# Kernel tuning notes

Hardware: AMD Instinct MI355X
Metric: run time of the kernel (lower is better)

Reference implementation:

```python
import jax, jax.numpy as jnp
import numpy as np
import math

STRIDE = ((2, 2), (4, 4), (8, 8), (16, 16))  # (ws, hs) pairs
D_MODEL = 256
B, H, W = 8, 128, 128
BN_EPS = 1e-5
LEAKY_SLOPE = 0.2


def setup_inputs() -> dict:
    key = jax.random.key(0)
    ks = jax.random.split(key, 8)
    s = 1.0 / math.sqrt(D_MODEL)
    s3 = 1.0 / math.sqrt(D_MODEL * 9)
    return {
        "x": jax.random.normal(ks[0], (B, D_MODEL, H, W), jnp.float32),
        "wq": jax.random.normal(ks[1], (D_MODEL, D_MODEL, 1, 1), jnp.float32) * s,
        "bq": jnp.zeros((D_MODEL,), jnp.float32),
        "wk": jax.random.normal(ks[2], (D_MODEL, D_MODEL, 1, 1), jnp.float32) * s,
        "bk": jnp.zeros((D_MODEL,), jnp.float32),
        "wv": jax.random.normal(ks[3], (D_MODEL, D_MODEL, 1, 1), jnp.float32) * s,
        "bv": jnp.zeros((D_MODEL,), jnp.float32),
        "wo": jax.random.normal(ks[4], (D_MODEL, D_MODEL, 3, 3), jnp.float32) * s3,
        "bo": jnp.zeros((D_MODEL,), jnp.float32),
        "gamma": jnp.ones((D_MODEL,), jnp.float32),
        "beta": jnp.zeros((D_MODEL,), jnp.float32),
    }


def _conv1x1(x, w, bias):
    # 1x1 conv == channel matmul
    return jnp.einsum('bchw,oc->bohw', x, w[:, :, 0, 0]) + bias[None, :, None, None]


def reference(x, wq, bq, wk, bk, wv, bv, wo, bo, gamma, beta):
    b, c, h, w = x.shape
    n = len(STRIDE)
    d_k = c // n
    q = _conv1x1(x, wq, bq)
    k = _conv1x1(x, wk, bk)
    v = _conv1x1(x, wv, bv)
    outs = []
    for idx, (ws, hs) in enumerate(STRIDE):
        lo = idx * d_k
        oh, ow = h // hs, w // ws

        def gather(t):
            # strided patch gather: element (i,j) head <- t[:, :, i::hs, j::ws]
            t = t[:, lo:lo + d_k].reshape(b, d_k, oh, hs, ow, ws)
            return t.transpose(0, 3, 5, 1, 2, 4).reshape(b, hs * ws, d_k * oh * ow)

        qi, ki, vi = gather(q), gather(k), gather(v)
        scale = 1.0 / jnp.sqrt(jnp.asarray(qi.shape[-1], qi.dtype))
        scores = jnp.einsum('bsd,btd->bst', qi, ki) * scale  # [b, hs*ws, hs*ws]
        p = jax.nn.softmax(scores, axis=-1)
        y = jnp.einsum('bst,btd->bsd', p, vi)
        # scatter back exactly as the torch permute(0,3,1,4,2,5): h = i*oh + row
        y = y.reshape(b, hs, ws, d_k, oh, ow).transpose(0, 3, 1, 4, 2, 5).reshape(b, d_k, h, w)
        outs.append(y)
    out = jnp.concatenate(outs, axis=1)  # [b, c, h, w]
    # output_linear: 3x3 conv -> BatchNorm2d (training-mode batch stats) -> LeakyReLU(0.2)
    out = jax.lax.conv_general_dilated(out, wo, (1, 1), 'SAME',
                                       dimension_numbers=('NCHW', 'OIHW', 'NCHW'))
    out = out + bo[None, :, None, None]
    mean = out.mean(axis=(0, 2, 3))
    var = out.var(axis=(0, 2, 3))
    out = (out - mean[None, :, None, None]) * jax.lax.rsqrt(var[None, :, None, None] + BN_EPS)
    out = out * gamma[None, :, None, None] + beta[None, :, None, None]
    return jnp.where(out > 0, out, LEAKY_SLOPE * out)
```

## Files before the change

kernel.cpp:

```cpp
#include <hip/hip_runtime.h>
#include <stdint.h>


#define DEVI static __device__ __forceinline__

typedef short bf8 __attribute__((ext_vector_type(8)));
typedef float f32x4 __attribute__((ext_vector_type(4)));

DEVI unsigned short f2bf(float f) {
  unsigned u = __builtin_bit_cast(unsigned, f);
  u = (u + 0x7fffu + ((u >> 16) & 1u)) >> 16;
  return (unsigned short)u;
}
DEVI float bf2f(unsigned short h) {
  unsigned u = ((unsigned)h) << 16;
  return __builtin_bit_cast(float, u);
}

DEVI void gload16(const void* g, void* l) {
  __builtin_amdgcn_global_load_lds(
      (const __attribute__((address_space(1))) unsigned int*)g,
      (__attribute__((address_space(3))) unsigned int*)l, 16, 0, 0);
}

static const size_t WB_OFF  = 0;
static const size_t WOB_OFF = 393216;
static const size_t QN_OFF  = 1572864;
static const size_t KN_OFF  = QN_OFF + 67108864;
static const size_t VN_OFF  = KN_OFF + 67108864;
static const size_t YN_OFF  = VN_OFF + 67108864;
static const size_t SC_OFF  = YN_OFF + 67108864;
static const size_t PRB_OFF = SC_OFF + 2236928;
static const size_t BNP_OFF = PRB_OFF + 1118464;
static const size_t BNS_OFF = BNP_OFF + 4194304;
static const size_t ZP_OFF  = BNS_OFF + 2048;
static const size_t WS_NEED = ZP_OFF + 256;

__global__ void k_prep(const float* __restrict__ wq, const float* __restrict__ wk,
                       const float* __restrict__ wv, const float* __restrict__ wo,
                       unsigned short* __restrict__ Wb, unsigned short* __restrict__ Wob) {
  int i = blockIdx.x * 256 + threadIdx.x;
  if (i < 196608) {
    int z = i >> 16, r = i & 65535;
    const float* w = (z == 0) ? wq : (z == 1) ? wk : wv;
    Wb[i] = f2bf(w[r]);
  } else {
    int j = i - 196608;
    int o = j / 2304, k = j - o * 2304;
    int e = k >> 8, c = k & 255;
    Wob[j] = f2bf(wo[(o * 256 + c) * 9 + e]);
  }
}

__global__ void k_zero(float* __restrict__ p, int n) {
  int i = blockIdx.x * 256 + threadIdx.x;
  for (; i < n; i += gridDim.x * 256) p[i] = 0.f;
}

__global__ __launch_bounds__(256) void k_qkv(
    const float* __restrict__ x, const unsigned short* __restrict__ Wb,
    const float* __restrict__ bq, const float* __restrict__ bk, const float* __restrict__ bv,
    unsigned short* __restrict__ Qn, unsigned short* __restrict__ Kn,
    unsigned short* __restrict__ Vn) {
  const int pt = blockIdx.x, b = blockIdx.y;
  const int p0 = pt * 64;
  const int tid = threadIdx.x;

  __shared__ __align__(16) unsigned short xt[64 * 256];
  __shared__ __align__(16) unsigned short ot[64 * 256];

  const float* xb = x + (size_t)b * 256 * 16384;
  for (int k = 0; k < 16; ++k) {
    int i = tid + k * 256;
    int c = i >> 4, p4 = (i & 15) * 4;
    float4 v = *(const float4*)(xb + (size_t)c * 16384 + p0 + p4);
    xt[(p4 + 0) * 256 + (c ^ (((p4 + 0) & 7) << 3))] = f2bf(v.x);
    xt[(p4 + 1) * 256 + (c ^ (((p4 + 1) & 7) << 3))] = f2bf(v.y);
    xt[(p4 + 2) * 256 + (c ^ (((p4 + 2) & 7) << 3))] = f2bf(v.z);
    xt[(p4 + 3) * 256 + (c ^ (((p4 + 3) & 7) << 3))] = f2bf(v.w);
  }
  __syncthreads();

  const int wave = tid >> 6, lane = tid & 63;
  const int lr = lane & 15, lk = lane >> 4;
  const int obase = wave * 64;

  for (int z = 0; z < 3; ++z) {
    const unsigned short* Wz = Wb + (size_t)z * 65536;
    f32x4 acc[4][4];
    for (int m = 0; m < 4; ++m)
      for (int n = 0; n < 4; ++n)
        for (int r = 0; r < 4; ++r) acc[m][n][r] = 0.f;

    for (int ks = 0; ks < 8; ++ks) {
      int c0 = ks * 32 + lk * 8;
      bf8 a[4], bb[4];
#pragma unroll
      for (int m = 0; m < 4; ++m)
        a[m] = *(const bf8*)(Wz + (size_t)(obase + m * 16 + lr) * 256 + c0);
#pragma unroll
      for (int n = 0; n < 4; ++n) {
        int p = n * 16 + lr;
        bb[n] = *(const bf8*)(&xt[p * 256 + (c0 ^ ((p & 7) << 3))]);
      }
#pragma unroll
      for (int m = 0; m < 4; ++m)
#pragma unroll
        for (int n = 0; n < 4; ++n)
          acc[m][n] = __builtin_amdgcn_mfma_f32_16x16x32_bf16(a[m], bb[n], acc[m][n], 0, 0, 0);
    }

    const float* bias = (z == 0) ? bq : (z == 1) ? bk : bv;
    unsigned short* On = (z == 0) ? Qn : (z == 1) ? Kn : Vn;
    __syncthreads();
#pragma unroll
    for (int m = 0; m < 4; ++m) {
      int ob4 = obase + m * 16 + lk * 4;
      float4 b4 = *(const float4*)(bias + ob4);
#pragma unroll
      for (int n = 0; n < 4; ++n) {
        int p = n * 16 + lr;
        ushort4 v4;
        v4.x = f2bf(acc[m][n][0] + b4.x);
        v4.y = f2bf(acc[m][n][1] + b4.y);
        v4.z = f2bf(acc[m][n][2] + b4.z);
        v4.w = f2bf(acc[m][n][3] + b4.w);
        *(ushort4*)(&ot[p * 256 + (ob4 ^ ((p & 7) << 3))]) = v4;
      }
    }
    __syncthreads();
    unsigned short* gb = On + ((size_t)b * 16384 + p0) * 256;
#pragma unroll
    for (int i = 0; i < 8; ++i) {
      int ch = tid + i * 256;
      *(uint4*)(gb + ch * 8) = *(const uint4*)(&ot[ch * 8]);
    }
  }
}

template <int IDX>
__global__ __launch_bounds__(256) void k_gram(
    const unsigned short* __restrict__ Qn, const unsigned short* __restrict__ Kn,
    float* __restrict__ scores) {
  constexpr int HS = 2 << IDX, S = HS * HS, OH = 64 >> IDX, NSP = OH * OH;
  constexpr int SPW = (IDX == 2) ? 2 : 8;
  constexpr int DSUB = SPW * 64;
  constexpr int SPB = NSP / 32;
  constexpr int STEPS = SPB / SPW;
  constexpr int ROWS = S;
  constexpr int TPT = S * SPW * 8 / 256;
  constexpr int SCOFF = (IDX == 0) ? 0 : (IDX == 1) ? 128 : 2176;
  constexpr int HC = IDX * 64;
  constexpr int MT = (IDX == 2) ? 4 : 1;

  const int chk = blockIdx.x, b = blockIdx.y;
  const int tid = threadIdx.x;
  const int wave = tid >> 6, lane = tid & 63, lr = lane & 15, lk = lane >> 4;

  __shared__ __align__(16) unsigned short qg[ROWS * DSUB];
  __shared__ __align__(16) unsigned short kg[ROWS * DSUB];
  __shared__ float red[S * S];

  const size_t base = (size_t)b * 16384 * 256;

  f32x4 acc[MT][MT];
  for (int m = 0; m < MT; ++m)
    for (int n = 0; n < MT; ++n)
      for (int r = 0; r < 4; ++r) acc[m][n][r] = 0.f;

  for (int st = 0; st < STEPS; ++st) {
    const int sp0 = chk * SPB + st * SPW;
    __syncthreads();
#pragma unroll
    for (int r = 0; r < TPT; ++r) {
      int task = tid + r * 256;
      int cg = task & 7, pl = task >> 3;
      int spl = pl >> (2 * (IDX + 1)), s = pl & (S - 1);
      int sp = sp0 + spl;
      int ohi = sp >> (6 - IDX), owi = sp & (OH - 1);
      int ii = s >> (IDX + 1), jj = s & (HS - 1);
      int p = (ohi * HS + ii) * 128 + owi * HS + jj;
      size_t gaddr = base + (size_t)p * 256 + HC + ((cg ^ (p & 7)) << 3);
      int laddr = s * DSUB + (((spl * 8 + cg) ^ (s & 7)) << 3);
      *(uint4*)(qg + laddr) = *(const uint4*)(Qn + gaddr);
      *(uint4*)(kg + laddr) = *(const uint4*)(Kn + gaddr);
    }
    __syncthreads();
    if (IDX == 2) {
      int kgid = wave * 4 + lk;
      bf8 a[4], bb[4];
#pragma unroll
      for (int m = 0; m < 4; ++m) {
        int row = m * 16 + lr;
        int off = row * DSUB + ((kgid ^ (row & 7)) << 3);
        a[m] = *(const bf8*)(qg + off);
        bb[m] = *(const bf8*)(kg + off);
      }
#pragma unroll
      for (int m = 0; m < 4; ++m)
#pragma unroll
        for (int n = 0; n < 4; ++n)
          acc[m][n] = __builtin_amdgcn_mfma_f32_16x16x32_bf16(a[m], bb[n], acc[m][n], 0, 0, 0);
    } else {
      int row = lr & (ROWS - 1);
#pragma unroll
      for (int kk = 0; kk < 4; ++kk) {
        int kgid = (wave * 4 + kk) * 4 + lk;
        int off = row * DSUB + ((kgid ^ (row & 7)) << 3);
        bf8 a = *(const bf8*)(qg + off);
        bf8 bb = *(const bf8*)(kg + off);
        acc[0][0] = __builtin_amdgcn_mfma_f32_16x16x32_bf16(a, bb, acc[0][0], 0, 0, 0);
      }
    }
  }

  __syncthreads();
  for (int i2 = tid; i2 < S * S; i2 += 256) red[i2] = 0.f;
  __syncthreads();
  if (IDX == 2) {
#pragma unroll
    for (int m = 0; m < 4; ++m)
#pragma unroll
      for (int n = 0; n < 4; ++n)
#pragma unroll
        for (int r = 0; r < 4; ++r)
          atomicAdd(&red[(m * 16 + lk * 4 + r) * 64 + n * 16 + lr], acc[m][n][r]);
  } else if (IDX == 1) {
#pragma unroll
    for (int r = 0; r < 4; ++r)
      atomicAdd(&red[(lk * 4 + r) * 16 + lr], acc[0][0][r]);
  } else {
    if (lk == 0 && lr < 4) {
#pragma unroll
      for (int r = 0; r < 4; ++r)
        atomicAdd(&red[r * 4 + lr], acc[0][0][r]);
    }
  }
  __syncthreads();
  float* sc = scores + SCOFF + (size_t)b * S * S;
  for (int i2 = tid; i2 < S * S; i2 += 256) atomicAdd(sc + i2, red[i2]);
}

__global__ __launch_bounds__(256) void k_gram3(
    const unsigned short* __restrict__ Qn, const unsigned short* __restrict__ Kn,
    float* __restrict__ part3) {
  const int qc = blockIdx.x, tq = blockIdx.y, b = blockIdx.z;
  const int tid = threadIdx.x;
  const int wave = tid >> 6, lane = tid & 63, lr = lane & 15, lk = lane >> 4;

  __shared__ __align__(16) unsigned short qg[256 * 64];
  __shared__ __align__(16) unsigned short kg[64 * 64];

  const size_t base = (size_t)b * 16384 * 256;

  f32x4 acc[4][4];
  for (int m = 0; m < 4; ++m)
    for (int n = 0; n < 4; ++n)
      for (int r = 0; r < 4; ++r) acc[m][n][r] = 0.f;

  for (int st = 0; st < 8; ++st) {
    int sp = qc * 8 + st;
    int ohi = sp >> 3, owi = sp & 7;
    __syncthreads();
#pragma unroll
    for (int r = 0; r < 8; ++r) {
      int task = tid + r * 256;
      int cg = task & 7, s = task >> 3;
      int p = (ohi * 16 + (s >> 4)) * 128 + owi * 16 + (s & 15);
      uint4 v = *(const uint4*)(Qn + base + (size_t)p * 256 + 192 + ((cg ^ (p & 7)) << 3));
      *(uint4*)(qg + s * 64 + ((cg ^ (s & 7)) << 3)) = v;
    }
#pragma unroll
    for (int r = 0; r < 2; ++r) {
      int task = tid + r * 256;
      int cg = task & 7, tl = task >> 3;
      int p = (ohi * 16 + tq * 4 + (tl >> 4)) * 128 + owi * 16 + (tl & 15);
      uint4 v = *(const uint4*)(Kn + base + (size_t)p * 256 + 192 + ((cg ^ (p & 7)) << 3));
      *(uint4*)(kg + tl * 64 + ((cg ^ (tl & 7)) << 3)) = v;
    }
    __syncthreads();
#pragma unroll
    for (int kk = 0; kk < 2; ++kk) {
      int kgid = kk * 4 + lk;
      bf8 a[4], bb[4];
#pragma unroll
      for (int m = 0; m < 4; ++m) {
        int row = wave * 64 + m * 16 + lr;
        a[m] = *(const bf8*)(qg + row * 64 + ((kgid ^ (row & 7)) << 3));
      }
#pragma unroll
      for (int n = 0; n < 4; ++n) {
        int rowb = n * 16 + lr;
        bb[n] = *(const bf8*)(kg + rowb * 64 + ((kgid ^ (rowb & 7)) << 3));
      }
#pragma unroll
      for (int m = 0; m < 4; ++m)
#pragma unroll
        for (int n = 0; n < 4; ++n)
          acc[m][n] = __builtin_amdgcn_mfma_f32_16x16x32_bf16(a[m], bb[n], acc[m][n], 0, 0, 0);
    }
  }

  float* pb = part3 + (((size_t)qc * 8 + b) * 65536);
#pragma unroll
  for (int m = 0; m < 4; ++m)
#pragma unroll
    for (int r = 0; r < 4; ++r) {
      int srow = wave * 64 + m * 16 + lk * 4 + r;
#pragma unroll
      for (int n = 0; n < 4; ++n)
        pb[srow * 256 + tq * 64 + n * 16 + lr] = acc[m][n][r];
    }
}

__global__ __launch_bounds__(256) void k_softmax(const float* __restrict__ scores,
                                                 unsigned short* __restrict__ prb) {
  const int idx = blockIdx.x, b = blockIdx.y;
  const int S = 4 << (2 * idx);
  const int off = (idx == 0 ? 0 : idx == 1 ? 128 : 2176) + b * S * S;
  const int s = threadIdx.x;
  if (s >= S) return;
  const float scale = rsqrtf(64.0f * (float)(4096 >> (2 * idx)));
  const float* row = scores + off + s * S;
  float m = -1e30f;
  for (int t = 0; t < S; ++t) m = fmaxf(m, row[t]);
  m *= scale;
  float sum = 0.f;
  for (int t = 0; t < S; ++t) sum += __expf(row[t] * scale - m);
  float inv = 1.0f / sum;
  unsigned short* prow = prb + off + s * S;
  for (int t = 0; t < S; ++t) prow[t] = f2bf(__expf(row[t] * scale - m) * inv);
}

__global__ __launch_bounds__(256) void k_softmax3(const float* __restrict__ part3,
                                                  unsigned short* __restrict__ prb) {
  const int sc_ = blockIdx.x, b = blockIdx.y;
  const int tid = threadIdx.x;
  const int s = sc_ * 32 + (tid >> 3);
  const int t0 = (tid & 7) * 32;
  float v[32];
#pragma unroll
  for (int k = 0; k < 32; ++k) v[k] = 0.f;
  for (int q = 0; q < 8; ++q) {
    const float4* pp = (const float4*)(part3 + (((size_t)q * 8 + b) * 256 + s) * 256 + t0);
#pragma unroll
    for (int k = 0; k < 8; ++k) {
      float4 u = pp[k];
      v[k * 4 + 0] += u.x; v[k * 4 + 1] += u.y; v[k * 4 + 2] += u.z; v[k * 4 + 3] += u.w;
    }
  }
  const float scale = 1.0f / 64.0f;
  float m = -1e30f;
#pragma unroll
  for (int k = 0; k < 32; ++k) { v[k] *= scale; m = fmaxf(m, v[k]); }
  m = fmaxf(m, __shfl_xor(m, 1));
  m = fmaxf(m, __shfl_xor(m, 2));
  m = fmaxf(m, __shfl_xor(m, 4));
  float sum = 0.f;
#pragma unroll
  for (int k = 0; k < 32; ++k) { v[k] = __expf(v[k] - m); sum += v[k]; }
  sum += __shfl_xor(sum, 1);
  sum += __shfl_xor(sum, 2);
  sum += __shfl_xor(sum, 4);
  float inv = 1.0f / sum;
  unsigned short* prw = prb + 34944 + (size_t)b * 65536 + s * 256 + t0;
#pragma unroll
  for (int k8 = 0; k8 < 4; ++k8) {
    unsigned short tmp[8];
#pragma unroll
    for (int e = 0; e < 8; ++e) tmp[e] = f2bf(v[k8 * 8 + e] * inv);
    *(uint4*)(prw + k8 * 8) = *(const uint4*)tmp;
  }
}

template <int IDX>
__global__ __launch_bounds__(256) void k_pv(
    const unsigned short* __restrict__ Vn, const unsigned short* __restrict__ prb,
    unsigned short* __restrict__ Yn) {
  constexpr int HS = 2 << IDX, S = HS * HS, OH = 64 >> IDX;
  constexpr int IT = (IDX == 0) ? 8 : (IDX == 1) ? 4 : 1;
  constexpr int POFF = (IDX == 0) ? 0 : (IDX == 1) ? 128 : 2176;
  const int bx = blockIdx.x, b = blockIdx.y;
  const int c = threadIdx.x & 63, spg = threadIdx.x >> 6;
  __shared__ __align__(16) float pl[S * S];
  const unsigned short* pr = prb + POFF + (size_t)b * S * S;
  for (int i = threadIdx.x; i < S * S; i += 256) pl[i] = bf2f(pr[i]);
  __syncthreads();
  const int hc = IDX * 64;
  const unsigned short* vb = Vn + (size_t)b * 16384 * 256;
  unsigned short* yb = Yn + (size_t)b * 16384 * 256;
  for (int it = 0; it < IT; ++it) {
    int sp = bx * (4 * IT) + it * 4 + spg;
    int ohi = sp >> (6 - IDX), owi = sp & (OH - 1);
    float v[S];
#pragma unroll
    for (int t = 0; t < S; ++t) {
      int po = (ohi * HS + t / HS) * 128 + owi * HS + (t % HS);
      v[t] = bf2f(vb[(size_t)po * 256 + ((hc + c) ^ ((po & 7) << 3))]);
    }
    for (int s = 0; s < S; ++s) {
      const float4* p4 = (const float4*)(pl + s * S);
      float a = 0.f;
#pragma unroll
      for (int t4 = 0; t4 < S / 4; ++t4) {
        float4 pp = p4[t4];
        a += pp.x * v[t4 * 4] + pp.y * v[t4 * 4 + 1] + pp.z * v[t4 * 4 + 2] + pp.w * v[t4 * 4 + 3];
      }
      int po = ((s >> (IDX + 1)) * OH + ohi) * 128 + (s & (HS - 1)) * OH + owi;
      yb[(size_t)po * 256 + ((hc + c) ^ ((po & 7) << 3))] = f2bf(a);
    }
  }
}

__global__ __launch_bounds__(256) void k_pv3(
    const unsigned short* __restrict__ Vn, const unsigned short* __restrict__ prb,
    unsigned short* __restrict__ Yn) {
  const int sp = blockIdx.x, b = blockIdx.y;
  const int ohi = sp >> 3, owi = sp & 7;
  const int tid = threadIdx.x;
  __shared__ __align__(16) unsigned short vl[64 * 256];
  const unsigned short* vb = Vn + (size_t)b * 16384 * 256;
  {
    int t = tid;
    int po = (ohi * 16 + (t >> 4)) * 128 + owi * 16 + (t & 15);
    const unsigned short* src = vb + (size_t)po * 256;
    int xv = (po & 7) << 3;
#pragma unroll
    for (int g = 0; g < 8; ++g) {
      ushort4 lo = *(const ushort4*)(src + ((192 + g * 8) ^ xv));
      ushort4 hi = *(const ushort4*)(src + ((192 + g * 8) ^ xv) + 4);
      unsigned short vv[8] = {lo.x, lo.y, lo.z, lo.w, hi.x, hi.y, hi.z, hi.w};
#pragma unroll
      for (int e = 0; e < 8; ++e) {
        int cc = g * 8 + e;
        vl[cc * 256 + (t ^ ((cc & 7) << 3))] = vv[e];
      }
    }
  }
  __syncthreads();

  const int wave = tid >> 6, lane = tid & 63;
  const int lr = lane & 15, lk = lane >> 4;
  const int sb = wave * 64;
  const unsigned short* pr = prb + 34944 + (size_t)b * 65536;

  f32x4 acc[4][4];
  for (int m = 0; m < 4; ++m)
    for (int n = 0; n < 4; ++n)
      for (int r = 0; r < 4; ++r) acc[m][n][r] = 0.f;

  for (int kk = 0; kk < 8; ++kk) {
    int t0 = kk * 32 + lk * 8;
    bf8 a[4], bb[4];
#pragma unroll
    for (int m = 0; m < 4; ++m)
      a[m] = *(const bf8*)(pr + (size_t)(sb + m * 16 + lr) * 256 + t0);
#pragma unroll
    for (int n = 0; n < 4; ++n) {
      int cc = n * 16 + lr;
      bb[n] = *(const bf8*)(&vl[cc * 256 + (t0 ^ ((cc & 7) << 3))]);
    }
#pragma unroll
    for (int m = 0; m < 4; ++m)
#pragma unroll
      for (int n = 0; n < 4; ++n)
        acc[m][n] = __builtin_amdgcn_mfma_f32_16x16x32_bf16(a[m], bb[n], acc[m][n], 0, 0, 0);
  }

  unsigned short* yb = Yn + (size_t)b * 16384 * 256;
#pragma unroll
  for (int m = 0; m < 4; ++m) {
#pragma unroll
    for (int r = 0; r < 4; ++r) {
      int s = sb + m * 16 + lk * 4 + r;
      int si = s >> 4, sj = s & 15;
      int po = (si * 8 + ohi) * 128 + sj * 8 + owi;
#pragma unroll
      for (int n = 0; n < 4; ++n) {
        int cc = 192 + n * 16 + lr;
        yb[(size_t)po * 256 + (cc ^ (owi << 3))] = f2bf(acc[m][n][r]);
      }
    }
  }
}

__global__ __launch_bounds__(512, 2) void k_conv(
    const unsigned short* __restrict__ Yn, const unsigned short* __restrict__ Wob,
    const float* __restrict__ bo, const unsigned short* __restrict__ zp,
    float* __restrict__ out, float* __restrict__ bnp) {
  __shared__ __align__(16) unsigned short ldsA[2][16384];
  __shared__ __align__(16) unsigned short ldsB[2][16384];

  const int bid = blockIdx.x;
  const int swz = (bid & 7) * 64 + (bid >> 3);
  const int b = swz >> 6, tile = swz & 63;
  const int y0 = (tile >> 3) * 16, x0 = (tile & 7) * 16;
  const int tid = threadIdx.x;
  const int wave = tid >> 6, lane = tid & 63;
  const int lr = lane & 15, lk = lane >> 4;
  const int wm = wave >> 2, wn = wave & 3;

  const unsigned short* yb = Yn + (size_t)b * 16384 * 256;

  auto STAGE = [&](int buf, int st) {
    int e = st >> 2;
    int dy = e / 3 - 1, dx = e % 3 - 1;
    int c0 = (st & 3) * 64, g0 = (st & 3) * 8;
#pragma unroll
    for (int i = 0; i < 4; ++i) {
      int task = (wave * 4 + i) * 64 + lane;
      int o = task >> 3, cg = task & 7;
      const unsigned short* sa = Wob + o * 2304 + e * 256 + c0 + ((cg ^ (o & 7)) << 3);
      gload16(sa, &ldsA[buf][(wave * 4 + i) * 512]);
      int py = o >> 4, px = o & 15;
      int h = y0 + py + dy, w = x0 + px + dx;
      const unsigned short* sb;
      if (h >= 0 && h < 128 && w >= 0 && w < 128) {
        int pp = h * 128 + w;
        int gl = (cg ^ (o & 7)) ^ (pp & 7);
        sb = yb + (size_t)pp * 256 + ((g0 + gl) << 3);
      } else {
        sb = zp;
      }
      gload16(sb, &ldsB[buf][(wave * 4 + i) * 512]);
    }
  };

  f32x4 acc[8][4];
#pragma unroll
  for (int m = 0; m < 8; ++m)
#pragma unroll
    for (int n = 0; n < 4; ++n)
#pragma unroll
      for (int r = 0; r < 4; ++r) acc[m][n][r] = 0.f;

  int cur = 0;
  STAGE(0, 0);
  for (int t = 0; t < 36; ++t) {
    if (t < 35) {
      STAGE(cur ^ 1, t + 1);
      asm volatile("s_waitcnt vmcnt(8)" ::: "memory");
    } else {
      asm volatile("s_waitcnt vmcnt(0)" ::: "memory");
    }
    __builtin_amdgcn_s_barrier();
    asm volatile("" ::: "memory");
#pragma unroll
    for (int kk = 0; kk < 2; ++kk) {
      int kg = kk * 4 + lk;
      bf8 a[8], bf[4];
#pragma unroll
      for (int m = 0; m < 8; ++m) {
        int row = wm * 128 + m * 16 + lr;
        a[m] = *(const bf8*)(&ldsA[cur][row * 64 + ((kg ^ (row & 7)) << 3)]);
      }
#pragma unroll
      for (int n = 0; n < 4; ++n) {
        int rn = wn * 64 + n * 16 + lr;
        bf[n] = *(const bf8*)(&ldsB[cur][rn * 64 + ((kg ^ (rn & 7)) << 3)]);
      }
#pragma unroll
      for (int m = 0; m < 8; ++m)
#pragma unroll
        for (int n = 0; n < 4; ++n)
          acc[m][n] = __builtin_amdgcn_mfma_f32_16x16x32_bf16(a[m], bf[n], acc[m][n], 0, 0, 0);
    }
    asm volatile("" ::: "memory");
    __builtin_amdgcn_s_barrier();
    cur ^= 1;
  }

  float* ob = out + (size_t)b * 256 * 16384;
  float* red1 = (float*)&ldsA[0][0];
  float* red2 = red1 + 1024;
#pragma unroll
  for (int m = 0; m < 8; ++m) {
#pragma unroll
    for (int r = 0; r < 4; ++r) {
      int o = wm * 128 + m * 16 + lk * 4 + r;
      float bvv = bo[o];
      float s1 = 0.f, s2 = 0.f;
#pragma unroll
      for (int n = 0; n < 4; ++n) {
        int pix = wn * 64 + n * 16 + lr;
        int py = pix >> 4, px = pix & 15;
        float v = acc[m][n][r] + bvv;
        ob[(size_t)o * 16384 + (y0 + py) * 128 + x0 + px] = v;
        s1 += v;
        s2 += v * v;
      }
      for (int off = 1; off < 16; off <<= 1) {
        s1 += __shfl_xor(s1, off, 64);
        s2 += __shfl_xor(s2, off, 64);
      }
      if (lr == 0) {
        int ol = m * 16 + lk * 4 + r;
        red1[wave * 128 + ol] = s1;
        red2[wave * 128 + ol] = s2;
      }
    }
  }
  __syncthreads();
  {
    int o = tid & 255, stat = tid >> 8;
    int wm2 = o >> 7, ol = o & 127;
    const float* rd = stat ? red2 : red1;
    float s = rd[(wm2 * 4 + 0) * 128 + ol] + rd[(wm2 * 4 + 1) * 128 + ol] +
              rd[(wm2 * 4 + 2) * 128 + ol] + rd[(wm2 * 4 + 3) * 128 + ol];
    bnp[((size_t)(b * 64 + tile) * 256 + o) * 2 + stat] = s;
  }
}

__global__ __launch_bounds__(256) void k_bnred(
    const float* __restrict__ bnp, const float* __restrict__ gamma,
    const float* __restrict__ beta, float* __restrict__ bns) {
  const int o = blockIdx.x;
  const int tid = threadIdx.x;
  float s1 = 0.f, s2 = 0.f;
  for (int k = tid; k < 512; k += 256) {
    s1 += bnp[((size_t)k * 256 + o) * 2 + 0];
    s2 += bnp[((size_t)k * 256 + o) * 2 + 1];
  }
  __shared__ float r1[256], r2[256];
  r1[tid] = s1; r2[tid] = s2;
  __syncthreads();
  for (int off = 128; off > 0; off >>= 1) {
    if (tid < off) { r1[tid] += r1[tid + off]; r2[tid] += r2[tid + off]; }
    __syncthreads();
  }
  if (tid == 0) {
    const float cnt = 8.0f * 16384.0f;
    float mean = r1[0] / cnt;
    float var = r2[0] / cnt - mean * mean;
    float sc = gamma[o] * rsqrtf(var + 1e-5f);
    bns[o] = sc;
    bns[256 + o] = beta[o] - mean * sc;
  }
}

__global__ void k_bnapply(float* __restrict__ out, const float* __restrict__ bns) {
  size_t i = ((size_t)blockIdx.x * 256 + threadIdx.x) * 4;
  const size_t total = 33554432;
  const size_t stride = (size_t)gridDim.x * 256 * 4;
  for (; i < total; i += stride) {
    float4 v = *(float4*)(out + i);
    int o = (int)((i >> 14) & 255);
    float sc = bns[o], shv = bns[256 + o];
    v.x = v.x * sc + shv; v.x = v.x > 0.f ? v.x : 0.2f * v.x;
    v.y = v.y * sc + shv; v.y = v.y > 0.f ? v.y : 0.2f * v.y;
    v.z = v.z * sc + shv; v.z = v.z > 0.f ? v.z : 0.2f * v.z;
    v.w = v.w * sc + shv; v.w = v.w > 0.f ? v.w : 0.2f * v.w;
    *(float4*)(out + i) = v;
  }
}

extern "C" void kernel_launch(void* const* d_in, const int* in_sizes, int n_in,
                              void* d_out, int out_size, void* d_ws, size_t ws_size,
                              hipStream_t stream) {
  if (ws_size < WS_NEED) return;

  const float* x     = (const float*)d_in[0];
  const float* wq    = (const float*)d_in[1];
  const float* bq    = (const float*)d_in[2];
  const float* wk    = (const float*)d_in[3];
  const float* bk    = (const float*)d_in[4];
  const float* wv    = (const float*)d_in[5];
  const float* bv    = (const float*)d_in[6];
  const float* wo    = (const float*)d_in[7];
  const float* bo    = (const float*)d_in[8];
  const float* gamma = (const float*)d_in[9];
  const float* beta  = (const float*)d_in[10];
  float* out = (float*)d_out;
  char* ws = (char*)d_ws;

  unsigned short* Wb  = (unsigned short*)(ws + WB_OFF);
  unsigned short* Wob = (unsigned short*)(ws + WOB_OFF);
  unsigned short* Qn  = (unsigned short*)(ws + QN_OFF);
  unsigned short* Kn  = (unsigned short*)(ws + KN_OFF);
  unsigned short* Vn  = (unsigned short*)(ws + VN_OFF);
  unsigned short* Yn  = (unsigned short*)(ws + YN_OFF);
  float* part3 = (float*)(ws + YN_OFF);
  float* scores = (float*)(ws + SC_OFF);
  unsigned short* prb = (unsigned short*)(ws + PRB_OFF);
  float* bnp    = (float*)(ws + BNP_OFF);
  float* bns    = (float*)(ws + BNS_OFF);
  unsigned short* zp = (unsigned short*)(ws + ZP_OFF);

  k_prep<<<dim3(3072), dim3(256), 0, stream>>>(wq, wk, wv, wo, Wb, Wob);
  k_zero<<<dim3(137), dim3(256), 0, stream>>>(scores, 34944);
  k_zero<<<dim3(1), dim3(64), 0, stream>>>((float*)zp, 64);
  k_qkv<<<dim3(256, 8), dim3(256), 0, stream>>>(x, Wb, bq, bk, bv, Qn, Kn, Vn);
  k_gram<0><<<dim3(32, 8), dim3(256), 0, stream>>>(Qn, Kn, scores);
  k_gram<1><<<dim3(32, 8), dim3(256), 0, stream>>>(Qn, Kn, scores);
  k_gram<2><<<dim3(32, 8), dim3(256), 0, stream>>>(Qn, Kn, scores);
  k_gram3<<<dim3(8, 4, 8), dim3(256), 0, stream>>>(Qn, Kn, part3);
  k_softmax<<<dim3(3, 8), dim3(256), 0, stream>>>(scores, prb);
  k_softmax3<<<dim3(8, 8), dim3(256), 0, stream>>>(part3, prb);
  k_pv<0><<<dim3(128, 8), dim3(256), 0, stream>>>(Vn, prb, Yn);
  k_pv<1><<<dim3(64, 8), dim3(256), 0, stream>>>(Vn, prb, Yn);
  k_pv<2><<<dim3(64, 8), dim3(256), 0, stream>>>(Vn, prb, Yn);
  k_pv3<<<dim3(64, 8), dim3(256), 0, stream>>>(Vn, prb, Yn);
  k_conv<<<dim3(512), dim3(512), 0, stream>>>(Yn, Wob, bo, zp, out, bnp);
  k_bnred<<<dim3(256), dim3(256), 0, stream>>>(bnp, gamma, beta, bns);
  k_bnapply<<<dim3(4096), dim3(256), 0, stream>>>(out, bns);
}
```

Before: 613.3 us.

## Split conv K-tiles into quarter sub-tiles with an 8-slot LDS ring pipeline

Restructures the 3x3 conv GEMM main loop. The old double-buffered 256x256x64 stage is split into four half-tile LDS slots (two A halves, two B halves) inside an 8-slot ring, with loads issued five sub-stages ahead. Each sub-step computes one quadrant of the accumulator tile, and MFMA sections are wrapped in s_setprio. The aim is to deepen prefetch and overlap global-to-LDS loads with MFMA at finer granularity, at the cost of more barriers per K-step and more complex bookkeeping.

```diff
diff --git a/kernel.cpp b/kernel.cpp
--- a/kernel.cpp
+++ b/kernel.cpp
@@ -488,8 +488,7 @@
     const unsigned short* __restrict__ Yn, const unsigned short* __restrict__ Wob,
     const float* __restrict__ bo, const unsigned short* __restrict__ zp,
     float* __restrict__ out, float* __restrict__ bnp) {
-  __shared__ __align__(16) unsigned short ldsA[2][16384];
-  __shared__ __align__(16) unsigned short ldsB[2][16384];
+  __shared__ __align__(16) unsigned short lds[8][8192];
 
   const int bid = blockIdx.x;
   const int swz = (bid & 7) * 64 + (bid >> 3);
@@ -499,30 +498,36 @@
   const int wave = tid >> 6, lane = tid & 63;
   const int lr = lane & 15, lk = lane >> 4;
   const int wm = wave >> 2, wn = wave & 3;
+  const int cg = lane & 7;
 
   const unsigned short* yb = Yn + (size_t)b * 16384 * 256;
 
-  auto STAGE = [&](int buf, int st) {
-    int e = st >> 2;
-    int dy = e / 3 - 1, dx = e % 3 - 1;
-    int c0 = (st & 3) * 64, g0 = (st & 3) * 8;
-#pragma unroll
-    for (int i = 0; i < 4; ++i) {
-      int task = (wave * 4 + i) * 64 + lane;
-      int o = task >> 3, cg = task & 7;
-      const unsigned short* sa = Wob + o * 2304 + e * 256 + c0 + ((cg ^ (o & 7)) << 3);
-      gload16(sa, &ldsA[buf][(wave * 4 + i) * 512]);
-      int py = o >> 4, px = o & 15;
-      int h = y0 + py + dy, w = x0 + px + dx;
-      const unsigned short* sb;
-      if (h >= 0 && h < 128 && w >= 0 && w < 128) {
-        int pp = h * 128 + w;
-        int gl = (cg ^ (o & 7)) ^ (pp & 7);
-        sb = yb + (size_t)pp * 256 + ((g0 + gl) << 3);
-      } else {
-        sb = zp;
-      }
-      gload16(sb, &ldsB[buf][(wave * 4 + i) * 512]);
+  auto STAGE = [&](int slot, int w, int KT) {
+    if (w < 2) {
+      const unsigned short* wsrc = Wob + (KT >> 2) * 256 + (KT & 3) * 64;
+#pragma unroll
+      for (int j = 0; j < 2; ++j) {
+        int rp = (wave * 2 + j) * 8 + (lane >> 3);
+        int o = ((rp >> 6) & 1) * 128 + w * 64 + (rp & 63);
+        int kg = cg ^ (rp & 7);
+        gload16(wsrc + o * 2304 + (kg << 3), &lds[slot][(wave * 2 + j) * 512]);
+      }
+    } else {
+      int e = KT >> 2;
+      int dy = e / 3 - 1, dx = e % 3 - 1, c8 = (KT & 3) * 8;
+#pragma unroll
+      for (int j = 0; j < 2; ++j) {
+        int rp = (wave * 2 + j) * 8 + (lane >> 3);
+        int n = ((rp >> 5) & 3) * 64 + (w - 2) * 32 + (rp & 31);
+        int kg = cg ^ (rp & 7);
+        int h = y0 + (n >> 4) + dy, ww = x0 + (n & 15) + dx;
+        const unsigned short* src = zp;
+        if (h >= 0 && h < 128 && ww >= 0 && ww < 128) {
+          int pp = h * 128 + ww;
+          src = yb + (size_t)pp * 256 + ((c8 + (kg ^ (pp & 7))) << 3);
+        }
+        gload16(src, &lds[slot][(wave * 2 + j) * 512]);
+      }
     }
   };
 
@@ -534,44 +539,57 @@
 #pragma unroll
       for (int r = 0; r < 4; ++r) acc[m][n][r] = 0.f;
 
-  int cur = 0;
-  STAGE(0, 0);
-  for (int t = 0; t < 36; ++t) {
-    if (t < 35) {
-      STAGE(cur ^ 1, t + 1);
-      asm volatile("s_waitcnt vmcnt(8)" ::: "memory");
-    } else {
-      asm volatile("s_waitcnt vmcnt(0)" ::: "memory");
-    }
-    __builtin_amdgcn_s_barrier();
-    asm volatile("" ::: "memory");
-#pragma unroll
-    for (int kk = 0; kk < 2; ++kk) {
-      int kg = kk * 4 + lk;
-      bf8 a[8], bf[4];
-#pragma unroll
-      for (int m = 0; m < 8; ++m) {
-        int row = wm * 128 + m * 16 + lr;
-        a[m] = *(const bf8*)(&ldsA[cur][row * 64 + ((kg ^ (row & 7)) << 3)]);
-      }
-#pragma unroll
-      for (int n = 0; n < 4; ++n) {
-        int rn = wn * 64 + n * 16 + lr;
-        bf[n] = *(const bf8*)(&ldsB[cur][rn * 64 + ((kg ^ (rn & 7)) << 3)]);
-      }
-#pragma unroll
-      for (int m = 0; m < 8; ++m)
-#pragma unroll
-        for (int n = 0; n < 4; ++n)
-          acc[m][n] = __builtin_amdgcn_mfma_f32_16x16x32_bf16(a[m], bf[n], acc[m][n], 0, 0, 0);
-    }
-    asm volatile("" ::: "memory");
-    __builtin_amdgcn_s_barrier();
-    cur ^= 1;
-  }
-
+  STAGE(0, 0, 0); STAGE(1, 1, 0); STAGE(2, 2, 0); STAGE(3, 3, 0); STAGE(4, 0, 1);
+
+  for (int gg = 0; gg < 18; ++gg) {
+#pragma unroll
+    for (int sub = 0; sub < 8; ++sub) {
+      const int g = sub >> 2;
+      const int r = sub & 3;
+      const int P = gg * 8 + sub;
+      if (P <= 138) {
+        STAGE((sub + 5) & 7, (sub + 5) & 3, gg * 2 + ((sub + 5) >> 2));
+        asm volatile("s_waitcnt vmcnt(6)" ::: "memory");
+      } else if (P == 140) {
+        asm volatile("s_waitcnt vmcnt(0)" ::: "memory");
+      }
+      __builtin_amdgcn_s_barrier();
+      asm volatile("" ::: "memory");
+      const int mh = r >> 1, nh = r & 1;
+      const int sA = g * 4 + mh, sB = g * 4 + 2 + nh;
+      bf8 a[4][2], bq2[2][2];
+#pragma unroll
+      for (int m2 = 0; m2 < 4; ++m2) {
+        int row = wm * 64 + m2 * 16 + lr;
+#pragma unroll
+        for (int kk = 0; kk < 2; ++kk)
+          a[m2][kk] = *(const bf8*)(&lds[sA][row * 64 + (((kk * 4 + lk) ^ (row & 7)) << 3)]);
+      }
+#pragma unroll
+      for (int n2 = 0; n2 < 2; ++n2) {
+        int row = wn * 32 + n2 * 16 + lr;
+#pragma unroll
+        for (int kk = 0; kk < 2; ++kk)
+          bq2[n2][kk] = *(const bf8*)(&lds[sB][row * 64 + (((kk * 4 + lk) ^ (row & 7)) << 3)]);
+      }
+      __builtin_amdgcn_s_setprio(1);
+#pragma unroll
+      for (int kk = 0; kk < 2; ++kk)
+#pragma unroll
+        for (int m2 = 0; m2 < 4; ++m2)
+#pragma unroll
+          for (int n2 = 0; n2 < 2; ++n2)
+            acc[mh * 4 + m2][nh * 2 + n2] = __builtin_amdgcn_mfma_f32_16x16x32_bf16(
+                a[m2][kk], bq2[n2][kk], acc[mh * 4 + m2][nh * 2 + n2], 0, 0, 0);
+      __builtin_amdgcn_s_setprio(0);
+      asm volatile("" ::: "memory");
+      __builtin_amdgcn_s_barrier();
+    }
+  }
+
+  __syncthreads();
   float* ob = out + (size_t)b * 256 * 16384;
-  float* red1 = (float*)&ldsA[0][0];
+  float* red1 = (float*)&lds[0][0];
   float* red2 = red1 + 1024;
 #pragma unroll
   for (int m = 0; m < 8; ++m) {
```

After: 591.7 us. -3.5%, faster.
